# Performance work log

Measured on AMD Instinct MI355X. Metric: run time of the kernel, lower is better.

## Reference

```python
import jax, jax.numpy as jnp
import numpy as np

BATCH, C, IMG, P = 32, 3, 224, 32
G = IMG // P            # 7
N = G * G               # 49 patches
E, NH, L = 768, 12, 12
DH = E // NH
DFF, MLP, NC = 3072, 2048, 5
FLAT = (N + 1 + L) * E  # 62*768 = 47616


def setup_inputs() -> dict:
    key = jax.random.key(0)
    ks = iter(jax.random.split(key, 32))
    nrm = lambda shape, s=0.02: jax.random.normal(next(ks), shape, jnp.float32) * s
    return {
        "x": jax.random.normal(next(ks), (BATCH, C, IMG, IMG), jnp.float32),
        "Wp": nrm((E, C, P, P)), "bp": jnp.zeros((E,), jnp.float32),
        "cls_token": jnp.zeros((1, 1, E), jnp.float32),
        "pos_embed": nrm((E, G + 1, G + 1)),  # overwritten by normal init in torch code
        "W_bb": nrm((C, E)), "b_bb": jnp.zeros((E,), jnp.float32),
        "Wqkv": nrm((L, 3 * E, E)), "bqkv": jnp.zeros((L, 3 * E), jnp.float32),
        "Wo": nrm((L, E, E)), "bo": jnp.zeros((L, E), jnp.float32),
        "ln1_s": jnp.ones((L, E), jnp.float32), "ln1_b": jnp.zeros((L, E), jnp.float32),
        "W1": nrm((L, DFF, E)), "b1": jnp.zeros((L, DFF), jnp.float32),
        "W2": nrm((L, E, DFF)), "b2": jnp.zeros((L, E), jnp.float32),
        "ln2_s": jnp.ones((L, E), jnp.float32), "ln2_b": jnp.zeros((L, E), jnp.float32),
        "lnf_s": jnp.ones((E,), jnp.float32), "lnf_b": jnp.zeros((E,), jnp.float32),
        "Wh1": nrm((MLP, FLAT)), "bh1": jnp.zeros((MLP,), jnp.float32),
        "Wh2": nrm((NC, MLP)), "bh2": jnp.zeros((NC,), jnp.float32),
    }


def _ln(x, s, b, eps=1e-5):
    mu = x.mean(-1, keepdims=True)
    var = ((x - mu) ** 2).mean(-1, keepdims=True)
    return (x - mu) * jax.lax.rsqrt(var + eps) * s + b


def reference(x, Wp, bp, cls_token, pos_embed, W_bb, b_bb,
              Wqkv, bqkv, Wo, bo, ln1_s, ln1_b, W1, b1, W2, b2, ln2_s, ln2_b,
              lnf_s, lnf_b, Wh1, bh1, Wh2, bh2):
    B = x.shape[0]
    # backbone stub: global average pool + linear -> [B, E]
    ximg = x.mean((2, 3)) @ W_bb + b_bb
    # patch embedding (importance weights are all ones -> subdivision branch is dead;
    # equivalent to strided conv, row-major patch order)
    xr = x.reshape(B, C, G, P, G, P)
    emb = jnp.einsum('bcipjq,ecpq->beij', xr, Wp) + bp[None, :, None, None]  # [B,E,G,G]
    patches = emb.reshape(B, E, N).transpose(0, 2, 1)                       # [B,N,E]
    h = jnp.concatenate([jnp.broadcast_to(cls_token, (B, 1, E)), patches], axis=1)
    pe = pos_embed.reshape(1, -1, E)[:, :h.shape[1], :]
    h = h + pe
    inv_sqrt_dh = 1.0 / np.sqrt(DH)
    for i in range(L):  # post-norm transformer encoder layer (relu FFN), seq grows each iter
        S = h.shape[1]
        qkv = h @ Wqkv[i].T + bqkv[i]
        q, k, v = jnp.split(qkv, 3, axis=-1)
        q = q.reshape(B, S, NH, DH)
        k = k.reshape(B, S, NH, DH)
        v = v.reshape(B, S, NH, DH)
        att = jax.nn.softmax(jnp.einsum('bqhd,bkhd->bhqk', q, k) * inv_sqrt_dh, axis=-1)
        o = jnp.einsum('bhqk,bkhd->bqhd', att, v).reshape(B, S, E) @ Wo[i].T + bo[i]
        h = _ln(h + o, ln1_s[i], ln1_b[i])
        ff = jax.nn.relu(h @ W1[i].T + b1[i]) @ W2[i].T + b2[i]
        h = _ln(h + ff, ln2_s[i], ln2_b[i])
        h = jnp.concatenate([ximg[:, None, :], h], axis=1)  # prepend backbone token
    h = _ln(h, lnf_s, lnf_b)
    h = h.reshape(B, -1)  # [B, (N+1+L)*E]
    out = jax.nn.gelu(h @ Wh1.T + bh1, approximate=False) @ Wh2.T + bh2
    return out
```

## Files before the change

### kernel.cpp

```cpp
#include <hip/hip_runtime.h>
#include <math.h>

#define B_ 32
#define C_ 3
#define IMG_ 224
#define P_ 32
#define G_ 7
#define NPATCH 49
#define E_ 768
#define NH_ 12
#define L_ 12
#define DFF_ 3072
#define MLP_ 2048
#define NC_ 5
#define TOK 62
#define MROWS (B_*TOK)
#define FLAT_ (TOK*E_)
#define MPAD 2048
#define PMROWS (B_*NPATCH)
#define PMPAD 1664
#define HKS 31
#define HKC (FLAT_/HKS)

typedef __bf16 bf16x8 __attribute__((ext_vector_type(8)));
typedef float f32x4 __attribute__((ext_vector_type(4)));

__device__ inline unsigned short f2bf(float f) {
    unsigned u = __float_as_uint(f);
    u += 0x7FFF + ((u >> 16) & 1);
    return (unsigned short)(u >> 16);
}

__device__ inline unsigned cvtpk(float lo, float hi) {
    unsigned r;
    asm("v_cvt_pk_bf16_f32 %0, %1, %2" : "=v"(r) : "v"(lo), "v"(hi));
    return r;
}

#define GLDS(gsrc, ldst) __builtin_amdgcn_global_load_lds( \
    (__attribute__((address_space(1))) const void*)(gsrc), \
    (__attribute__((address_space(3))) void*)(ldst), 16, 0, 0)

__global__ __launch_bounds__(256) void gemm_mfma(
    const unsigned short* __restrict__ A, const float* __restrict__ W,
    const float* __restrict__ bias, float* __restrict__ Cf, unsigned short* __restrict__ Cb,
    float* __restrict__ part, int M, int N, int K, int KC, int act)
{
    __shared__ unsigned short As[128 * 64];
    __shared__ unsigned short Bs[64 * 72];
    int tid = threadIdx.x;
    int m0 = blockIdx.y * 128, n0 = blockIdx.x * 64;
    int z = blockIdx.z;
    int kbeg = z * KC;
    int wid = tid >> 6, lane = tid & 63;
    int wm = wid >> 1, wn = wid & 1;
    int lr = lane & 15, lg = lane >> 4;
    int sr = tid >> 3, sc = (tid & 7) * 8;
    int brow = tid >> 2, bq = (tid & 3) * 16;

    f32x4 acc[4][2];
    #pragma unroll
    for (int mi = 0; mi < 4; ++mi)
        #pragma unroll
        for (int ni = 0; ni < 2; ++ni)
            acc[mi][ni] = (f32x4){0.f, 0.f, 0.f, 0.f};

    for (int k0 = kbeg; k0 < kbeg + KC; k0 += 64) {
        const float* bsrc = &W[(size_t)(n0 + brow) * K + k0 + bq];
        float4 bv0 = *reinterpret_cast<const float4*>(bsrc);
        float4 bv1 = *reinterpret_cast<const float4*>(bsrc + 4);
        float4 bv2 = *reinterpret_cast<const float4*>(bsrc + 8);
        float4 bv3 = *reinterpret_cast<const float4*>(bsrc + 12);
        #pragma unroll
        for (int t = 0; t < 4; ++t)
            GLDS(&A[(size_t)(m0 + sr + t * 32) * K + k0 + sc], &As[(sr + t * 32) * 64 + sc]);
        {
            uint4 u0, u1;
            u0.x = cvtpk(bv0.x, bv0.y); u0.y = cvtpk(bv0.z, bv0.w);
            u0.z = cvtpk(bv1.x, bv1.y); u0.w = cvtpk(bv1.z, bv1.w);
            u1.x = cvtpk(bv2.x, bv2.y); u1.y = cvtpk(bv2.z, bv2.w);
            u1.z = cvtpk(bv3.x, bv3.y); u1.w = cvtpk(bv3.z, bv3.w);
            *reinterpret_cast<uint4*>(&Bs[brow * 72 + bq]) = u0;
            *reinterpret_cast<uint4*>(&Bs[brow * 72 + bq + 8]) = u1;
        }
        __syncthreads();
        #pragma unroll
        for (int ks = 0; ks < 64; ks += 32) {
            bf16x8 af[4], bfr[2];
            #pragma unroll
            for (int mi = 0; mi < 4; ++mi)
                af[mi] = *reinterpret_cast<const bf16x8*>(&As[(wm * 64 + mi * 16 + lr) * 64 + ks + lg * 8]);
            #pragma unroll
            for (int ni = 0; ni < 2; ++ni)
                bfr[ni] = *reinterpret_cast<const bf16x8*>(&Bs[(wn * 32 + ni * 16 + lr) * 72 + ks + lg * 8]);
            #pragma unroll
            for (int mi = 0; mi < 4; ++mi)
                #pragma unroll
                for (int ni = 0; ni < 2; ++ni)
                    acc[mi][ni] = __builtin_amdgcn_mfma_f32_16x16x32_bf16(af[mi], bfr[ni], acc[mi][ni], 0, 0, 0);
        }
        __syncthreads();
    }

    bool split = (gridDim.z > 1);
    #pragma unroll
    for (int mi = 0; mi < 4; ++mi) {
        #pragma unroll
        for (int rr = 0; rr < 4; ++rr) {
            int row = m0 + wm * 64 + mi * 16 + lg * 4 + rr;
            #pragma unroll
            for (int ni = 0; ni < 2; ++ni) {
                int col = n0 + wn * 32 + ni * 16 + lr;
                float v = acc[mi][ni][rr];
                if (split) {
                    part[((size_t)z * M + row) * N + col] = v;
                } else {
                    v += bias[col];
                    if (act) v = fmaxf(v, 0.f);
                    if (Cb) Cb[(size_t)row * N + col] = f2bf(v);
                    else    Cf[(size_t)row * N + col] = v;
                }
            }
        }
    }
}

__global__ __launch_bounds__(256) void add_ln_fused(
    const float* __restrict__ h, const float* __restrict__ part, int nparts,
    const float* __restrict__ gb, const float* __restrict__ s, const float* __restrict__ bb,
    float* __restrict__ outf, unsigned short* __restrict__ outbf,
    const float* __restrict__ ximg, int tnew)
{
    int row = blockIdx.x;
    int t = row % TOK, b = row / TOK;
    int tid = threadIdx.x;
    if (t == tnew) {
        #pragma unroll
        for (int j = 0; j < 3; ++j) {
            int e = tid + j * 256;
            float v = ximg[b * E_ + e];
            if (outf)  outf[(size_t)row * E_ + e] = v;
            if (outbf) outbf[(size_t)row * E_ + e] = f2bf(v);
        }
        return;
    }
    __shared__ float sm[8];
    float v[3];
    #pragma unroll
    for (int j = 0; j < 3; ++j) {
        int e = tid + j * 256;
        float x = h[(size_t)row * E_ + e];
        for (int p = 0; p < nparts; ++p) x += part[((size_t)p * MPAD + row) * E_ + e];
        if (nparts) x += gb[e];
        v[j] = x;
    }
    float sum = v[0] + v[1] + v[2];
    #pragma unroll
    for (int o = 32; o >= 1; o >>= 1) sum += __shfl_xor(sum, o);
    int wid = tid >> 6, lane = tid & 63;
    if (lane == 0) sm[wid] = sum;
    __syncthreads();
    if (tid == 0) sm[0] = sm[0] + sm[1] + sm[2] + sm[3];
    __syncthreads();
    float mu = sm[0] * (1.0f / E_);
    __syncthreads();
    float sq = 0.f;
    #pragma unroll
    for (int j = 0; j < 3; ++j) { float d = v[j] - mu; sq += d * d; }
    #pragma unroll
    for (int o = 32; o >= 1; o >>= 1) sq += __shfl_xor(sq, o);
    if (lane == 0) sm[wid] = sq;
    __syncthreads();
    if (tid == 0) sm[0] = sm[0] + sm[1] + sm[2] + sm[3];
    __syncthreads();
    float rstd = rsqrtf(sm[0] * (1.0f / E_) + 1e-5f);
    #pragma unroll
    for (int j = 0; j < 3; ++j) {
        int e = tid + j * 256;
        float r = (v[j] - mu) * rstd * s[e] + bb[e];
        if (outf)  outf[(size_t)row * E_ + e] = r;
        if (outbf) outbf[(size_t)row * E_ + e] = f2bf(r);
    }
}

__global__ __launch_bounds__(256) void attn_mfma(
    const unsigned short* __restrict__ qkv, unsigned short* __restrict__ obf, int start)
{
    int h = blockIdx.x, b = blockIdx.y;
    int S = TOK - start;
    int tid = threadIdx.x;
    int wid = tid >> 6, lane = tid & 63;
    int lr = lane & 15, lg = lane >> 4;

    __shared__ unsigned short Qs[64 * 64];
    __shared__ unsigned short Ks[64 * 64];
    __shared__ unsigned short VT[64 * 72];
    __shared__ unsigned short Ps[4][16 * 72];

    const unsigned short* base = qkv + ((size_t)(b * TOK + start)) * 2304 + h * 64;

    #pragma unroll
    for (int t = 0; t < 2; ++t) {
        int r0 = wid * 16 + t * 8;
        int row = r0 + (lane >> 3);
        int sc = ((lane & 7) ^ (row & 7)) * 8;
        GLDS(base + (size_t)row * 2304 + sc,       &Qs[r0 * 64]);
        GLDS(base + (size_t)row * 2304 + 768 + sc, &Ks[r0 * 64]);
    }
    #pragma unroll
    for (int it = 0; it < 8; ++it) {
        int pi = it * 256 + tid;
        int k = pi >> 5;
        int d0 = (pi & 31) * 2;
        unsigned u = *reinterpret_cast<const unsigned*>(base + (size_t)k * 2304 + 1536 + d0);
        VT[d0 * 72 + k] = (unsigned short)(u & 0xffff);
        VT[(d0 + 1) * 72 + k] = (unsigned short)(u >> 16);
    }
    __syncthreads();

    f32x4 st[4];
    #pragma unroll
    for (int mt = 0; mt < 4; ++mt) st[mt] = (f32x4){0.f, 0.f, 0.f, 0.f};
    bf16x8 qb[2];
    #pragma unroll
    for (int ks = 0; ks < 2; ++ks) {
        int qrow = wid * 16 + lr;
        int ck = ((ks * 4 + lg) ^ (qrow & 7)) * 8;
        qb[ks] = *reinterpret_cast<const bf16x8*>(&Qs[qrow * 64 + ck]);
    }
    #pragma unroll
    for (int mt = 0; mt < 4; ++mt) {
        #pragma unroll
        for (int ks = 0; ks < 2; ++ks) {
            int krow = mt * 16 + lr;
            int ck = ((ks * 4 + lg) ^ (krow & 7)) * 8;
            bf16x8 kb = *reinterpret_cast<const bf16x8*>(&Ks[krow * 64 + ck]);
            st[mt] = __builtin_amdgcn_mfma_f32_16x16x32_bf16(kb, qb[ks], st[mt], 0, 0, 0);
        }
    }

    float mx = -1e30f;
    #pragma unroll
    for (int mt = 0; mt < 4; ++mt)
        #pragma unroll
        for (int rr = 0; rr < 4; ++rr) {
            int k = mt * 16 + lg * 4 + rr;
            float v = st[mt][rr] * 0.125f;
            v = (k < S) ? v : -1e30f;
            st[mt][rr] = v;
            mx = fmaxf(mx, v);
        }
    mx = fmaxf(mx, __shfl_xor(mx, 16));
    mx = fmaxf(mx, __shfl_xor(mx, 32));
    float sum = 0.f;
    #pragma unroll
    for (int mt = 0; mt < 4; ++mt)
        #pragma unroll
        for (int rr = 0; rr < 4; ++rr) {
            float p = __expf(st[mt][rr] - mx);
            st[mt][rr] = p;
            sum += p;
        }
    sum += __shfl_xor(sum, 16);
    sum += __shfl_xor(sum, 32);
    float inv = 1.0f / sum;

    #pragma unroll
    for (int mt = 0; mt < 4; ++mt) {
        int k0 = mt * 16 + lg * 4;
        unsigned u0 = cvtpk(st[mt][0] * inv, st[mt][1] * inv);
        unsigned u1 = cvtpk(st[mt][2] * inv, st[mt][3] * inv);
        *reinterpret_cast<unsigned*>(&Ps[wid][lr * 72 + k0]) = u0;
        *reinterpret_cast<unsigned*>(&Ps[wid][lr * 72 + k0 + 2]) = u1;
    }
    __syncthreads();

    f32x4 oa[4];
    #pragma unroll
    for (int nt = 0; nt < 4; ++nt) oa[nt] = (f32x4){0.f, 0.f, 0.f, 0.f};
    #pragma unroll
    for (int ks = 0; ks < 2; ++ks) {
        bf16x8 pa = *reinterpret_cast<const bf16x8*>(&Ps[wid][lr * 72 + ks * 32 + lg * 8]);
        #pragma unroll
        for (int nt = 0; nt < 4; ++nt) {
            bf16x8 vb = *reinterpret_cast<const bf16x8*>(&VT[(nt * 16 + lr) * 72 + ks * 32 + lg * 8]);
            oa[nt] = __builtin_amdgcn_mfma_f32_16x16x32_bf16(pa, vb, oa[nt], 0, 0, 0);
        }
    }

    #pragma unroll
    for (int nt = 0; nt < 4; ++nt)
        #pragma unroll
        for (int rr = 0; rr < 4; ++rr) {
            int qs = wid * 16 + lg * 4 + rr;
            if (qs < S)
                obf[((size_t)(b * TOK + start + qs)) * E_ + h * 64 + nt * 16 + lr] = f2bf(oa[nt][rr]);
        }
}

__global__ __launch_bounds__(256) void mean_kernel(const float* __restrict__ x, float* __restrict__ xmean)
{
    int bc = blockIdx.x;
    const float* p = x + (size_t)bc * IMG_ * IMG_;
    float s = 0.f;
    for (int i = threadIdx.x; i < IMG_ * IMG_; i += 256) s += p[i];
    #pragma unroll
    for (int o = 32; o >= 1; o >>= 1) s += __shfl_xor(s, o);
    __shared__ float sm[4];
    int wid = threadIdx.x >> 6, lane = threadIdx.x & 63;
    if (lane == 0) sm[wid] = s;
    __syncthreads();
    if (threadIdx.x == 0) xmean[bc] = (sm[0] + sm[1] + sm[2] + sm[3]) / (float)(IMG_ * IMG_);
}

__global__ void ximg_kernel(const float* __restrict__ xmean, const float* __restrict__ Wbb,
                            const float* __restrict__ bbb, float* __restrict__ ximg)
{
    int idx = blockIdx.x * 256 + threadIdx.x;
    if (idx >= B_ * E_) return;
    int e = idx % E_, b = idx / E_;
    ximg[idx] = xmean[b * 3 + 0] * Wbb[0 * E_ + e]
              + xmean[b * 3 + 1] * Wbb[1 * E_ + e]
              + xmean[b * 3 + 2] * Wbb[2 * E_ + e] + bbb[e];
}

__global__ void im2col_kernel(const float* __restrict__ x, unsigned short* __restrict__ Pm)
{
    int idx = (blockIdx.x * 256 + threadIdx.x) * 4;
    if (idx >= PMROWS * 3072) return;
    int k = idx % 3072;
    int rowp = idx / 3072;
    int n = rowp % NPATCH, b = rowp / NPATCH;
    int i = n / G_, j = n % G_;
    int c = k >> 10;
    int r = k & 1023;
    int p = r >> 5, q = r & 31;
    float4 v = *reinterpret_cast<const float4*>(
        &x[(((size_t)b * C_ + c) * IMG_ + i * P_ + p) * IMG_ + j * P_ + q]);
    ushort4 o;
    o.x = f2bf(v.x); o.y = f2bf(v.y); o.z = f2bf(v.z); o.w = f2bf(v.w);
    *reinterpret_cast<ushort4*>(&Pm[idx]) = o;
}

__global__ void build_h0_kernel(const float* __restrict__ part, const float* __restrict__ bp,
                                const float* __restrict__ cls, const float* __restrict__ pos,
                                float* __restrict__ hbuf, unsigned short* __restrict__ hbf)
{
    int idx = blockIdx.x * 256 + threadIdx.x;
    if (idx >= MROWS * E_) return;
    int e = idx % E_;
    int t = (idx / E_) % TOK;
    int b = idx / (E_ * TOK);
    float v = 0.f;
    if (t >= 12) {
        int sseq = t - 12;
        float base;
        if (sseq == 0) base = cls[e];
        else {
            int prow = b * NPATCH + (sseq - 1);
            base = bp[e];
            #pragma unroll
            for (int s = 0; s < 3; ++s) base += part[((size_t)s * PMPAD + prow) * E_ + e];
        }
        v = base + pos[sseq * E_ + e];
    }
    hbuf[idx] = v;
    hbf[idx] = f2bf(v);
}

__global__ __launch_bounds__(256) void head1_mfma(
    const unsigned short* __restrict__ hfb, const float* __restrict__ Wh1,
    float* __restrict__ part)
{
    int tid = threadIdx.x;
    int wid = tid >> 6, lane = tid & 63;
    int lr = lane & 15, lg = lane >> 4;
    int n0 = blockIdx.x * 64 + wid * 16;
    int kc = blockIdx.y;
    f32x4 acc0 = (f32x4){0.f, 0.f, 0.f, 0.f};
    f32x4 acc1 = (f32x4){0.f, 0.f, 0.f, 0.f};
    const float* wrow = Wh1 + (size_t)(n0 + lr) * FLAT_ + (size_t)kc * HKC + lg * 8;
    const unsigned short* a0 = hfb + (size_t)lr * FLAT_ + (size_t)kc * HKC + lg * 8;
    const unsigned short* a1 = hfb + (size_t)(16 + lr) * FLAT_ + (size_t)kc * HKC + lg * 8;
    #pragma unroll 4
    for (int k = 0; k < HKC; k += 32) {
        float4 w0 = *reinterpret_cast<const float4*>(wrow + k);
        float4 w1 = *reinterpret_cast<const float4*>(wrow + k + 4);
        uint4 u;
        u.x = cvtpk(w0.x, w0.y); u.y = cvtpk(w0.z, w0.w);
        u.z = cvtpk(w1.x, w1.y); u.w = cvtpk(w1.z, w1.w);
        bf16x8 bw = __builtin_bit_cast(bf16x8, u);
        bf16x8 af0 = *reinterpret_cast<const bf16x8*>(a0 + k);
        bf16x8 af1 = *reinterpret_cast<const bf16x8*>(a1 + k);
        acc0 = __builtin_amdgcn_mfma_f32_16x16x32_bf16(af0, bw, acc0, 0, 0, 0);
        acc1 = __builtin_amdgcn_mfma_f32_16x16x32_bf16(af1, bw, acc1, 0, 0, 0);
    }
    int n = n0 + lr;
    #pragma unroll
    for (int rr = 0; rr < 4; ++rr) {
        int m = lg * 4 + rr;
        part[((size_t)kc * B_ + m) * MLP_ + n] = acc0[rr];
        part[((size_t)kc * B_ + 16 + m) * MLP_ + n] = acc1[rr];
    }
}

__global__ void head1_fin_kernel(const float* __restrict__ part, const float* __restrict__ bh1,
                                 float* __restrict__ out1)
{
    int idx = blockIdx.x * 256 + threadIdx.x;
    if (idx >= B_ * MLP_) return;
    int n = idx % MLP_, b = idx / MLP_;
    float s = bh1[n];
    for (int kc = 0; kc < HKS; ++kc) s += part[((size_t)kc * B_ + b) * MLP_ + n];
    out1[idx] = 0.5f * s * (1.0f + erff(s * 0.70710678118654752f));
}

__global__ __launch_bounds__(256) void head2_kernel(const float* __restrict__ out1,
                                                    const float* __restrict__ Wh2,
                                                    const float* __restrict__ bh2,
                                                    float* __restrict__ out)
{
    int bc = blockIdx.x;
    int b = bc / NC_, c = bc % NC_;
    float s = 0.f;
    for (int nn = threadIdx.x; nn < MLP_; nn += 256) s += out1[(size_t)b * MLP_ + nn] * Wh2[(size_t)c * MLP_ + nn];
    #pragma unroll
    for (int o = 32; o >= 1; o >>= 1) s += __shfl_xor(s, o);
    __shared__ float sm[4];
    int wid = threadIdx.x >> 6, lane = threadIdx.x & 63;
    if (lane == 0) sm[wid] = s;
    __syncthreads();
    if (threadIdx.x == 0) out[bc] = sm[0] + sm[1] + sm[2] + sm[3] + bh2[c];
}

extern "C" void kernel_launch(void* const* d_in, const int* in_sizes, int n_in,
                              void* d_out, int out_size, void* d_ws, size_t ws_size,
                              hipStream_t stream)
{
    (void)in_sizes; (void)n_in; (void)out_size; (void)ws_size;
    const float* x    = (const float*)d_in[0];
    const float* Wp   = (const float*)d_in[1];
    const float* bp   = (const float*)d_in[2];
    const float* cls  = (const float*)d_in[3];
    const float* pos  = (const float*)d_in[4];
    const float* Wbb  = (const float*)d_in[5];
    const float* bbb  = (const float*)d_in[6];
    const float* Wqkv = (const float*)d_in[7];
    const float* bqkv = (const float*)d_in[8];
    const float* Wo   = (const float*)d_in[9];
    const float* bo   = (const float*)d_in[10];
    const float* ln1s = (const float*)d_in[11];
    const float* ln1b = (const float*)d_in[12];
    const float* W1   = (const float*)d_in[13];
    const float* b1   = (const float*)d_in[14];
    const float* W2   = (const float*)d_in[15];
    const float* b2   = (const float*)d_in[16];
    const float* ln2s = (const float*)d_in[17];
    const float* ln2b = (const float*)d_in[18];
    const float* lnfs = (const float*)d_in[19];
    const float* lnfb = (const float*)d_in[20];
    const float* Wh1  = (const float*)d_in[21];
    const float* bh1  = (const float*)d_in[22];
    const float* Wh2  = (const float*)d_in[23];
    const float* bh2  = (const float*)d_in[24];
    float* out = (float*)d_out;

    float* ws = (float*)d_ws;
    size_t off = 0;
    float* hbuf   = ws + off; off += (size_t)MROWS * E_;
    float* qslab  = ws + off; off += (size_t)3 * MPAD * E_;
    unsigned short* hbf  = (unsigned short*)(ws + off); off += (size_t)MPAD * E_ / 2;
    unsigned short* obf  = (unsigned short*)(ws + off); off += (size_t)MPAD * E_ / 2;
    unsigned short* ffbf = (unsigned short*)(ws + off); off += (size_t)MPAD * DFF_ / 2;
    unsigned short* hfb  = (unsigned short*)(ws + off); off += (size_t)MROWS * E_ / 2;
    float* ximg  = ws + off; off += B_ * E_;
    float* xmean = ws + off; off += 128;
    float* out1  = ws + off; off += B_ * MLP_;

    float* part = qslab;
    unsigned short* qkvb = (unsigned short*)qslab;
    unsigned short* Pmbf = ffbf;

    mean_kernel<<<B_ * C_, 256, 0, stream>>>(x, xmean);
    ximg_kernel<<<(B_ * E_ + 255) / 256, 256, 0, stream>>>(xmean, Wbb, bbb, ximg);

    im2col_kernel<<<(PMROWS * 3072 / 4 + 255) / 256, 256, 0, stream>>>(x, Pmbf);
    gemm_mfma<<<dim3(E_ / 64, PMPAD / 128, 3), 256, 0, stream>>>(
        Pmbf, Wp, nullptr, nullptr, nullptr, part, PMPAD, E_, 3072, 1024, 0);
    build_h0_kernel<<<(MROWS * E_ + 255) / 256, 256, 0, stream>>>(part, bp, cls, pos, hbuf, hbf);

    for (int i = 0; i < L_; ++i) {
        int start = 12 - i;
        gemm_mfma<<<dim3(2304 / 64, MPAD / 128, 1), 256, 0, stream>>>(
            hbf, Wqkv + (size_t)i * 2304 * E_, bqkv + i * 2304, nullptr, qkvb, nullptr, MPAD, 2304, E_, E_, 0);
        attn_mfma<<<dim3(NH_, B_), 256, 0, stream>>>(qkvb, obf, start);
        gemm_mfma<<<dim3(E_ / 64, MPAD / 128, 2), 256, 0, stream>>>(
            obf, Wo + (size_t)i * E_ * E_, nullptr, nullptr, nullptr, part, MPAD, E_, E_, 384, 0);
        add_ln_fused<<<MROWS, 256, 0, stream>>>(
            hbuf, part, 2, bo + i * E_, ln1s + i * E_, ln1b + i * E_, hbuf, hbf, nullptr, -1);
        gemm_mfma<<<dim3(DFF_ / 64, MPAD / 128, 1), 256, 0, stream>>>(
            hbf, W1 + (size_t)i * DFF_ * E_, b1 + i * DFF_, nullptr, ffbf, nullptr, MPAD, DFF_, E_, E_, 1);
        gemm_mfma<<<dim3(E_ / 64, MPAD / 128, 2), 256, 0, stream>>>(
            ffbf, W2 + (size_t)i * E_ * DFF_, nullptr, nullptr, nullptr, part, MPAD, E_, DFF_, 1536, 0);
        add_ln_fused<<<MROWS, 256, 0, stream>>>(
            hbuf, part, 2, b2 + i * E_, ln2s + i * E_, ln2b + i * E_, hbuf, hbf, ximg, 11 - i);
    }

    add_ln_fused<<<MROWS, 256, 0, stream>>>(
        hbuf, nullptr, 0, nullptr, lnfs, lnfb, nullptr, hfb, nullptr, -1);
    head1_mfma<<<dim3(MLP_ / 64, HKS), 256, 0, stream>>>(hfb, Wh1, part);
    head1_fin_kernel<<<(B_ * MLP_ + 255) / 256, 256, 0, stream>>>(part, bh1, out1);
    head2_kernel<<<B_ * NC_, 256, 0, stream>>>(out1, Wh2, bh2, out);
}
```

Before: 1.747 ms.

## Compact transformer GEMMs to the active token rows of each layer

The encoder layers previously ran every GEMM over all padded rows (B*62 padded to 2048), even though layer i only uses S = 50+i tokens per batch. The GEMMs now run over a compacted row count Mc = B*S padded to 128. A row map gathers the active rows of h, and attention, partial sums and layer norm index compact buffers. This removes the wasted FLOPs and bandwidth spent on inactive leading token slots, at the cost of per-row address arithmetic in the GEMM A-load and more index bookkeeping.

Measured after the change: 1.725 ms. No clear change (-1.2%).

```diff
diff --git a/kernel.cpp b/kernel.cpp
--- a/kernel.cpp
+++ b/kernel.cpp
@@ -44,7 +44,8 @@
 __global__ __launch_bounds__(256) void gemm_mfma(
     const unsigned short* __restrict__ A, const float* __restrict__ W,
     const float* __restrict__ bias, float* __restrict__ Cf, unsigned short* __restrict__ Cb,
-    float* __restrict__ part, int M, int N, int K, int KC, int act)
+    float* __restrict__ part, int Mc, int Mcp, int N, int K, int KC, int act,
+    int Smap, int tstart)
 {
     __shared__ unsigned short As[128 * 64];
     __shared__ unsigned short Bs[64 * 72];
@@ -58,6 +59,18 @@
     int sr = tid >> 3, sc = (tid & 7) * 8;
     int brow = tid >> 2, bq = (tid & 3) * 16;
 
+    const unsigned short* aptr[4];
+    #pragma unroll
+    for (int tt = 0; tt < 4; ++tt) {
+        int m_r = m0 + sr + tt * 32;
+        int grow;
+        if (Smap > 0) {
+            if (m_r < Mc) { int bb = m_r / Smap; grow = bb * TOK + tstart + (m_r - bb * Smap); }
+            else grow = 0;
+        } else grow = m_r;
+        aptr[tt] = A + (size_t)grow * K + sc;
+    }
+
     f32x4 acc[4][2];
     #pragma unroll
     for (int mi = 0; mi < 4; ++mi)
@@ -72,8 +85,8 @@
         float4 bv2 = *reinterpret_cast<const float4*>(bsrc + 8);
         float4 bv3 = *reinterpret_cast<const float4*>(bsrc + 12);
         #pragma unroll
-        for (int t = 0; t < 4; ++t)
-            GLDS(&A[(size_t)(m0 + sr + t * 32) * K + k0 + sc], &As[(sr + t * 32) * 64 + sc]);
+        for (int tt = 0; tt < 4; ++tt)
+            GLDS(aptr[tt] + k0, &As[(sr + tt * 32) * 64 + sc]);
         {
             uint4 u0, u1;
             u0.x = cvtpk(bv0.x, bv0.y); u0.y = cvtpk(bv0.z, bv0.w);
@@ -113,8 +126,8 @@
                 int col = n0 + wn * 32 + ni * 16 + lr;
                 float v = acc[mi][ni][rr];
                 if (split) {
-                    part[((size_t)z * M + row) * N + col] = v;
-                } else {
+                    part[((size_t)z * Mcp + row) * N + col] = v;
+                } else if (row < Mc) {
                     v += bias[col];
                     if (act) v = fmaxf(v, 0.f);
                     if (Cb) Cb[(size_t)row * N + col] = f2bf(v);
@@ -129,12 +142,14 @@
     const float* __restrict__ h, const float* __restrict__ part, int nparts,
     const float* __restrict__ gb, const float* __restrict__ s, const float* __restrict__ bb,
     float* __restrict__ outf, unsigned short* __restrict__ outbf,
-    const float* __restrict__ ximg, int tnew)
-{
-    int row = blockIdx.x;
-    int t = row % TOK, b = row / TOK;
+    const float* __restrict__ ximg, int t0, int span, int S, int tstart, int Mcp)
+{
+    int blk = blockIdx.x;
+    int b = blk / span, tl = blk - b * span;
+    int t = t0 + tl;
+    int row = b * TOK + t;
     int tid = threadIdx.x;
-    if (t == tnew) {
+    if (t < tstart) {
         #pragma unroll
         for (int j = 0; j < 3; ++j) {
             int e = tid + j * 256;
@@ -144,13 +159,14 @@
         }
         return;
     }
+    int crow = b * S + (t - tstart);
     __shared__ float sm[8];
     float v[3];
     #pragma unroll
     for (int j = 0; j < 3; ++j) {
         int e = tid + j * 256;
         float x = h[(size_t)row * E_ + e];
-        for (int p = 0; p < nparts; ++p) x += part[((size_t)p * MPAD + row) * E_ + e];
+        for (int p = 0; p < nparts; ++p) x += part[((size_t)p * Mcp + crow) * E_ + e];
         if (nparts) x += gb[e];
         v[j] = x;
     }
@@ -184,10 +200,9 @@
 }
 
 __global__ __launch_bounds__(256) void attn_mfma(
-    const unsigned short* __restrict__ qkv, unsigned short* __restrict__ obf, int start)
+    const unsigned short* __restrict__ qkv, unsigned short* __restrict__ obf, int S)
 {
     int h = blockIdx.x, b = blockIdx.y;
-    int S = TOK - start;
     int tid = threadIdx.x;
     int wid = tid >> 6, lane = tid & 63;
     int lr = lane & 15, lg = lane >> 4;
@@ -197,22 +212,24 @@
     __shared__ unsigned short VT[64 * 72];
     __shared__ unsigned short Ps[4][16 * 72];
 
-    const unsigned short* base = qkv + ((size_t)(b * TOK + start)) * 2304 + h * 64;
+    const unsigned short* qb_base = qkv + (size_t)h * 64;
 
     #pragma unroll
     for (int t = 0; t < 2; ++t) {
         int r0 = wid * 16 + t * 8;
         int row = r0 + (lane >> 3);
+        int rowg = (row < S) ? (b * S + row) : (b * S);
         int sc = ((lane & 7) ^ (row & 7)) * 8;
-        GLDS(base + (size_t)row * 2304 + sc,       &Qs[r0 * 64]);
-        GLDS(base + (size_t)row * 2304 + 768 + sc, &Ks[r0 * 64]);
+        GLDS(qb_base + (size_t)rowg * 2304 + sc,       &Qs[r0 * 64]);
+        GLDS(qb_base + (size_t)rowg * 2304 + 768 + sc, &Ks[r0 * 64]);
     }
     #pragma unroll
     for (int it = 0; it < 8; ++it) {
         int pi = it * 256 + tid;
         int k = pi >> 5;
+        int kg = (k < S) ? (b * S + k) : (b * S);
         int d0 = (pi & 31) * 2;
-        unsigned u = *reinterpret_cast<const unsigned*>(base + (size_t)k * 2304 + 1536 + d0);
+        unsigned u = *reinterpret_cast<const unsigned*>(qb_base + (size_t)kg * 2304 + 1536 + d0);
         VT[d0 * 72 + k] = (unsigned short)(u & 0xffff);
         VT[(d0 + 1) * 72 + k] = (unsigned short)(u >> 16);
     }
@@ -294,7 +311,7 @@
         for (int rr = 0; rr < 4; ++rr) {
             int qs = wid * 16 + lg * 4 + rr;
             if (qs < S)
-                obf[((size_t)(b * TOK + start + qs)) * E_ + h * 64 + nt * 16 + lr] = f2bf(oa[nt][rr]);
+                obf[((size_t)(b * S + qs)) * E_ + h * 64 + nt * 16 + lr] = f2bf(oa[nt][rr]);
         }
 }
 
@@ -486,28 +503,37 @@
 
     im2col_kernel<<<(PMROWS * 3072 / 4 + 255) / 256, 256, 0, stream>>>(x, Pmbf);
     gemm_mfma<<<dim3(E_ / 64, PMPAD / 128, 3), 256, 0, stream>>>(
-        Pmbf, Wp, nullptr, nullptr, nullptr, part, PMPAD, E_, 3072, 1024, 0);
+        Pmbf, Wp, nullptr, nullptr, nullptr, part, PMPAD, PMPAD, E_, 3072, 1024, 0, 0, 0);
     build_h0_kernel<<<(MROWS * E_ + 255) / 256, 256, 0, stream>>>(part, bp, cls, pos, hbuf, hbf);
 
     for (int i = 0; i < L_; ++i) {
         int start = 12 - i;
-        gemm_mfma<<<dim3(2304 / 64, MPAD / 128, 1), 256, 0, stream>>>(
-            hbf, Wqkv + (size_t)i * 2304 * E_, bqkv + i * 2304, nullptr, qkvb, nullptr, MPAD, 2304, E_, E_, 0);
-        attn_mfma<<<dim3(NH_, B_), 256, 0, stream>>>(qkvb, obf, start);
-        gemm_mfma<<<dim3(E_ / 64, MPAD / 128, 2), 256, 0, stream>>>(
-            obf, Wo + (size_t)i * E_ * E_, nullptr, nullptr, nullptr, part, MPAD, E_, E_, 384, 0);
-        add_ln_fused<<<MROWS, 256, 0, stream>>>(
-            hbuf, part, 2, bo + i * E_, ln1s + i * E_, ln1b + i * E_, hbuf, hbf, nullptr, -1);
-        gemm_mfma<<<dim3(DFF_ / 64, MPAD / 128, 1), 256, 0, stream>>>(
-            hbf, W1 + (size_t)i * DFF_ * E_, b1 + i * DFF_, nullptr, ffbf, nullptr, MPAD, DFF_, E_, E_, 1);
-        gemm_mfma<<<dim3(E_ / 64, MPAD / 128, 2), 256, 0, stream>>>(
-            ffbf, W2 + (size_t)i * E_ * DFF_, nullptr, nullptr, nullptr, part, MPAD, E_, DFF_, 1536, 0);
-        add_ln_fused<<<MROWS, 256, 0, stream>>>(
-            hbuf, part, 2, b2 + i * E_, ln2s + i * E_, ln2b + i * E_, hbuf, hbf, ximg, 11 - i);
+        int S = TOK - start;
+        int Mc = B_ * S;
+        int Mcp = ((Mc + 127) / 128) * 128;
+        gemm_mfma<<<dim3(2304 / 64, Mcp / 128, 1), 256, 0, stream>>>(
+            hbf, Wqkv + (size_t)i * 2304 * E_, bqkv + i * 2304, nullptr, qkvb, nullptr,
+            Mc, Mcp, 2304, E_, E_, 0, S, start);
+        attn_mfma<<<dim3(NH_, B_), 256, 0, stream>>>(qkvb, obf, S);
+        gemm_mfma<<<dim3(E_ / 64, Mcp / 128, 2), 256, 0, stream>>>(
+            obf, Wo + (size_t)i * E_ * E_, nullptr, nullptr, nullptr, part,
+            Mc, Mcp, E_, E_, 384, 0, 0, 0);
+        add_ln_fused<<<B_ * S, 256, 0, stream>>>(
+            hbuf, part, 2, bo + i * E_, ln1s + i * E_, ln1b + i * E_, hbuf, hbf,
+            nullptr, start, S, S, start, Mcp);
+        gemm_mfma<<<dim3(DFF_ / 64, Mcp / 128, 1), 256, 0, stream>>>(
+            hbf, W1 + (size_t)i * DFF_ * E_, b1 + i * DFF_, nullptr, ffbf, nullptr,
+            Mc, Mcp, DFF_, E_, E_, 1, S, start);
+        gemm_mfma<<<dim3(E_ / 64, Mcp / 128, 2), 256, 0, stream>>>(
+            ffbf, W2 + (size_t)i * E_ * DFF_, nullptr, nullptr, nullptr, part,
+            Mc, Mcp, E_, DFF_, 1536, 0, 0, 0);
+        add_ln_fused<<<B_ * (S + 1), 256, 0, stream>>>(
+            hbuf, part, 2, b2 + i * E_, ln2s + i * E_, ln2b + i * E_, hbuf, hbf,
+            ximg, start - 1, S + 1, S, start, Mcp);
     }
 
     add_ln_fused<<<MROWS, 256, 0, stream>>>(
-        hbuf, nullptr, 0, nullptr, lnfs, lnfb, nullptr, hfb, nullptr, -1);
+        hbuf, nullptr, 0, nullptr, lnfs, lnfb, nullptr, hfb, nullptr, 0, TOK, TOK, 0, 1);
     head1_mfma<<<dim3(MLP_ / 64, HKS), 256, 0, stream>>>(hfb, Wh1, part);
     head1_fin_kernel<<<(B_ * MLP_ + 255) / 256, 256, 0, stream>>>(part, bh1, out1);
     head2_kernel<<<B_ * NC_, 256, 0, stream>>>(out1, Wh2, bh2, out);
```
